# Performance work log

Hardware: AMD Instinct MI355X
Metric: run time of the kernel (lower is better)

The kernel has to match this reference:

```python
import jax, jax.numpy as jnp
import numpy as np

B, S, D = 2, 2048, 2048
H, D_NOPE, D_ROPE, D_V = 16, 128, 64, 128
R_Q, R_KV = 1536, 512
EPS = 1e-5


def _rmsnorm(x, w):
    return x * jax.lax.rsqrt(jnp.mean(x * x, axis=-1, keepdims=True) + EPS) * w


def setup_inputs() -> dict:
    key = jax.random.key(0)
    ks = jax.random.split(key, 12)
    x = jax.random.normal(ks[0], (B, S, D), jnp.float32)
    mask = jnp.zeros((B, 1, S, S), jnp.float32)  # unused by forward (is_causal)
    # NOTE: source apply_rope indexes freqs by HEAD axis -> shape (H, D_ROPE//2)
    ang = jax.random.uniform(ks[1], (H, D_ROPE // 2), jnp.float32) * (2.0 * np.pi)
    freqs_cos = jnp.cos(ang)
    freqs_sin = jnp.sin(ang)

    def lin(k, fan_in, fan_out):
        return jax.random.normal(k, (fan_in, fan_out), jnp.float32) * (fan_in ** -0.5)

    return {
        "x": x, "mask": mask, "freqs_cos": freqs_cos, "freqs_sin": freqs_sin,
        "w_cq": lin(ks[2], D, R_Q),
        "q_norm_w": jnp.ones((R_Q,), jnp.float32),
        "w_dq_nope": lin(ks[3], R_Q, H * D_NOPE),
        "w_dq_rope": lin(ks[4], R_Q, H * D_ROPE),
        "w_ckv": lin(ks[5], D, R_KV),
        "kv_norm_w": jnp.ones((R_KV,), jnp.float32),
        "w_dk_nope": lin(ks[6], R_KV, H * D_NOPE),
        "w_dv": lin(ks[7], R_KV, H * D_V),
        "w_k_rope": lin(ks[8], D, D_ROPE),
        "w_proj": lin(ks[9], H * D_V, D),
    }


def _apply_rope(q, k, cos, sin):
    # q: [B,H,S,Dr], k: [B,1,S,Dr]; cos/sin: [H, Dr/2] -> broadcast over head axis
    c = cos[None, :, None, :]
    s = sin[None, :, None, :]

    def rot(t):
        tr = t.reshape(t.shape[:-1] + (-1, 2))
        r, i = tr[..., 0], tr[..., 1]
        out_r = r * c - i * s  # k broadcasts from 1 head to H heads here
        out_i = r * s + i * c
        out = jnp.stack([out_r, out_i], axis=-1)
        return out.reshape(out.shape[:-2] + (-1,))

    return rot(q), rot(k)


def reference(x, mask, freqs_cos, freqs_sin, w_cq, q_norm_w, w_dq_nope, w_dq_rope,
              w_ckv, kv_norm_w, w_dk_nope, w_dv, w_k_rope, w_proj):
    b, s, _ = x.shape
    h = freqs_cos.shape[0]
    d_rope = freqs_cos.shape[1] * 2
    d_nope = w_dq_nope.shape[1] // h
    d_v = w_dv.shape[1] // h

    nq = _rmsnorm(x @ w_cq, q_norm_w)                      # [b,s,Rq]
    q_nope = (nq @ w_dq_nope).reshape(b, s, h, d_nope).transpose(0, 2, 1, 3)
    q_rope = (nq @ w_dq_rope).reshape(b, s, h, d_rope).transpose(0, 2, 1, 3)

    nkv = _rmsnorm(x @ w_ckv, kv_norm_w)                   # [b,s,Rkv]
    k_nope = (nkv @ w_dk_nope).reshape(b, s, h, d_nope).transpose(0, 2, 1, 3)
    v = (nkv @ w_dv).reshape(b, s, h, d_v).transpose(0, 2, 1, 3)
    v = v * (1.0 / jnp.sqrt(jnp.float32(h * d_v)))         # source scales V, not QK

    k_rope = (x @ w_k_rope).reshape(b, s, 1, d_rope).transpose(0, 2, 1, 3)
    q_rope, k_rope = _apply_rope(q_rope, k_rope, freqs_cos, freqs_sin)

    q = jnp.concatenate([q_nope, q_rope], axis=-1)         # [b,h,s,dn+dr]
    k = jnp.concatenate([k_nope, k_rope], axis=-1)

    attn_scale = 1.0 / jnp.sqrt(jnp.float32(d_nope + d_rope))  # SDPA default scale
    scores = jnp.einsum('bhqd,bhkd->bhqk', q, k) * attn_scale
    causal = jnp.tril(jnp.ones((s, s), dtype=bool))
    scores = jnp.where(causal[None, None], scores, -jnp.inf)
    probs = jax.nn.softmax(scores, axis=-1)

    out = jnp.einsum('bhqk,bhkd->bhqd', probs, v)
    out = out.transpose(0, 2, 1, 3).reshape(b, s, h * d_v)
    return out @ w_proj
```

## Files before the change

### kernel.cpp

```cpp
#include <hip/hip_runtime.h>
#include <hip/hip_bf16.h>
#include <cmath>
#include <cstdint>

using bf16 = __hip_bfloat16;
typedef __attribute__((ext_vector_type(8))) short short8;
typedef __attribute__((ext_vector_type(4))) float f32x4;

#define DEVINL static __device__ __forceinline__

DEVINL float bf2f(bf16 x) { return __bfloat162float(x); }
DEVINL bf16  f2bf(float x) { return __float2bfloat16(x); }
DEVINL unsigned short bfbits(float x) {
  bf16 h = __float2bfloat16(x);
  unsigned short u; __builtin_memcpy(&u, &h, 2); return u;
}
DEVINL float u2f(unsigned short u) {
  bf16 h; __builtin_memcpy(&h, &u, 2); return __bfloat162float(h);
}

typedef __attribute__((address_space(3))) void       lds_v;
typedef __attribute__((address_space(1))) const void gbl_v;
DEVINL void async16(const bf16* g, bf16* lds) {
  __builtin_amdgcn_global_load_lds((gbl_v*)g, (lds_v*)lds, 16, 0, 0);
}

template<int BM, int BN, int WM, int WN, bool OUT_BF16>
__global__ __launch_bounds__(256)
void gemm_bt(const bf16* __restrict__ A, const bf16* __restrict__ Bt,
             void* __restrict__ Cv, int M, int N, int K, float scale)
{
  constexpr int BK = 32;
  constexpr int FM = WM / 16, FN = WN / 16;
  constexpr int WAVES_N = BN / WN;
  __shared__ __align__(16) bf16 As[BM * BK];
  __shared__ __align__(16) bf16 Bs[BN * BK];

  const int tid = threadIdx.x, wid = tid >> 6, lane = tid & 63;
  const int nx = gridDim.x;
  const int nwg = nx * gridDim.y;
  const int bid0 = blockIdx.y * nx + blockIdx.x;
  const int cpx = nwg >> 3;
  const int swz = (bid0 & 7) * cpx + (bid0 >> 3);
  const int m0 = (swz / nx) * BM, n0 = (swz % nx) * BN;
  const int wm = wid / WAVES_N, wn = wid % WAVES_N;
  const int g = lane >> 4, l15 = lane & 15;
  const int srow = lane >> 2, schk = lane & 3;

  f32x4 acc[FM][FN] = {};

  for (int k0 = 0; k0 < K; k0 += BK) {
#pragma unroll
    for (int i = 0; i < BM / 64; i++) {
      int issue = wid * (BM / 64) + i;
      const bf16* src = A + (size_t)(m0 + issue * 16 + srow) * K + k0 + schk * 8;
      async16(src, (bf16*)As + issue * 512);
    }
#pragma unroll
    for (int i = 0; i < BN / 64; i++) {
      int issue = wid * (BN / 64) + i;
      const bf16* src = Bt + (size_t)(n0 + issue * 16 + srow) * K + k0 + schk * 8;
      async16(src, (bf16*)Bs + issue * 512);
    }
    __syncthreads();

    short8 af[FM], bfv[FN];
#pragma unroll
    for (int mi = 0; mi < FM; mi++)
      af[mi] = *(const short8*)&As[(wm * WM + mi * 16 + l15) * BK + g * 8];
#pragma unroll
    for (int ni = 0; ni < FN; ni++)
      bfv[ni] = *(const short8*)&Bs[(wn * WN + ni * 16 + l15) * BK + g * 8];
#pragma unroll
    for (int mi = 0; mi < FM; mi++)
#pragma unroll
      for (int ni = 0; ni < FN; ni++)
        acc[mi][ni] = __builtin_amdgcn_mfma_f32_16x16x32_bf16(af[mi], bfv[ni], acc[mi][ni], 0, 0, 0);
    __syncthreads();
  }

#pragma unroll
  for (int mi = 0; mi < FM; mi++)
#pragma unroll
    for (int ni = 0; ni < FN; ni++)
#pragma unroll
      for (int r = 0; r < 4; r++) {
        int row = m0 + wm * WM + mi * 16 + g * 4 + r;
        int col = n0 + wn * WN + ni * 16 + l15;
        float v = acc[mi][ni][r] * scale;
        if constexpr (OUT_BF16) ((bf16*)Cv)[(size_t)row * N + col] = f2bf(v);
        else                    ((float*)Cv)[(size_t)row * N + col] = v;
      }
}

struct TD { const float* src; bf16* dst; int R, C, start; float scale; };
struct TP8 { TD d[8]; };

__global__ void transpose_all_kernel(TP8 p)
{
  __shared__ float t[32][33];
  const int bid = blockIdx.x;
  int wi = 0;
#pragma unroll
  for (int i = 1; i < 8; i++) if (bid >= p.d[i].start) wi = i;
  const float* src = p.d[wi].src;
  bf16* dst = p.d[wi].dst;
  const int R = p.d[wi].R, C = p.d[wi].C;
  const float sc = p.d[wi].scale;
  const int local = bid - p.d[wi].start;
  const int ntx = C >> 5;
  const int bx = local % ntx, by = local / ntx;
  const int c0 = bx * 32, r0 = by * 32;
  const int tx = threadIdx.x, ty = threadIdx.y;
#pragma unroll
  for (int i = 0; i < 4; i++)
    t[ty + i * 8][tx] = src[(size_t)(r0 + ty + i * 8) * C + c0 + tx];
  __syncthreads();
#pragma unroll
  for (int i = 0; i < 4; i++)
    dst[(size_t)(c0 + ty + i * 8) * R + r0 + tx] = f2bf(t[tx][ty + i * 8] * sc);
}

__global__ void cast_kernel(const float* __restrict__ in, bf16* __restrict__ out, int n)
{
  int i = (blockIdx.x * 256 + threadIdx.x) * 4;
  if (i < n) {
    float4 v = *(const float4*)(in + i);
    ushort4 o;
    o.x = bfbits(v.x); o.y = bfbits(v.y); o.z = bfbits(v.z); o.w = bfbits(v.w);
    *reinterpret_cast<ushort4*>(out + i) = o;
  }
}

template<int NC>
__global__ __launch_bounds__(256)
void rmsnorm_kernel(const bf16* __restrict__ in, int stride, const float* __restrict__ w,
                    bf16* __restrict__ out)
{
  const int row = blockIdx.x;
  const bf16* x = in + (size_t)row * stride;
  float vals[NC / 256];
  float ssq = 0.f;
#pragma unroll
  for (int j = 0; j < NC / 512; j++) {
    int col = threadIdx.x * 2 + j * 512;
    ushort2 u = *reinterpret_cast<const ushort2*>(x + col);
    float a = u2f(u.x), c = u2f(u.y);
    vals[2 * j] = a; vals[2 * j + 1] = c;
    ssq += a * a + c * c;
  }
#pragma unroll
  for (int off = 32; off; off >>= 1) ssq += __shfl_xor(ssq, off, 64);
  __shared__ float red[4];
  const int wid = threadIdx.x >> 6, lane = threadIdx.x & 63;
  if (lane == 0) red[wid] = ssq;
  __syncthreads();
  float tot = red[0] + red[1] + red[2] + red[3];
  float sc = rsqrtf(tot * (1.f / NC) + 1e-5f);
#pragma unroll
  for (int j = 0; j < NC / 512; j++) {
    int col = threadIdx.x * 2 + j * 512;
    ushort2 o;
    o.x = bfbits(vals[2 * j] * sc * w[col]);
    o.y = bfbits(vals[2 * j + 1] * sc * w[col + 1]);
    *reinterpret_cast<ushort2*>(out + (size_t)row * NC + col) = o;
  }
}

__global__ void vtrans_kernel(const bf16* __restrict__ v, bf16* __restrict__ vt)
{
  __shared__ bf16 t[32][33];
  const int bh = blockIdx.z;
  const int s0 = blockIdx.x * 32, d0 = blockIdx.y * 32;
  const int tx = threadIdx.x, ty = threadIdx.y;
#pragma unroll
  for (int i = 0; i < 4; i++) {
    int s = s0 + ty + i * 8;
    t[ty + i * 8][tx] = v[((size_t)(bh >> 4) * 2048 + s) * 4096 + 2048 + (bh & 15) * 128 + d0 + tx];
  }
  __syncthreads();
#pragma unroll
  for (int i = 0; i < 4; i++)
    vt[((size_t)bh * 128 + d0 + ty + i * 8) * 2048 + s0 + tx] = t[tx][ty + i * 8];
}

__global__ __launch_bounds__(256, 2)
void flash_kernel(const bf16* __restrict__ qnr, const bf16* __restrict__ knb,
                  const bf16* __restrict__ krb, const bf16* __restrict__ vt,
                  bf16* __restrict__ o)
{
  constexpr int S = 2048, H = 16;
  constexpr int QSTR = 3072, KSTR = 4096, RSTR = 2112;
  const float SCALE = 0.07216878364870323f;
  const int bid = blockIdx.x;
  const int xcd = bid & 7, j = bid >> 3;
  const int slot = j & 31, rnd = j >> 5;
  const int grp = 4 * xcd + (slot >> 3);
  const int p = slot & 7;
  const int qti = rnd ? p : 15 - p;
  const int h = grp & 15, b = grp >> 4;
  const int q0 = qti * 128;

  const int tid = threadIdx.x, wid = tid >> 6, lane = tid & 63;
  const int g = lane >> 4, l15 = lane & 15;
  const int r4 = lane >> 4, s16 = lane & 15;
  const int r8 = lane >> 3, s8 = lane & 7;

  __shared__ __align__(16) bf16 KnS[2][64 * 128];
  __shared__ __align__(16) bf16 VtS[2][128 * 64];
  __shared__ __align__(16) bf16 KrS[64 * 64];
  __shared__ __align__(16) bf16 PS[4][16 * 64];

  short8 qf[2][6];
#pragma unroll
  for (int mi = 0; mi < 2; mi++) {
    int qrow = q0 + wid * 32 + mi * 16 + l15;
    const bf16* qnp = qnr + (size_t)(b * S + qrow) * QSTR + h * 128;
#pragma unroll
    for (int t = 0; t < 4; t++) qf[mi][t] = *(const short8*)(qnp + t * 32 + g * 8);
    const bf16* qrp = qnr + (size_t)(b * S + qrow) * QSTR + 2048 + h * 64;
#pragma unroll
    for (int t = 0; t < 2; t++) qf[mi][4 + t] = *(const short8*)(qrp + t * 32 + g * 8);
  }

  f32x4 oacc[2][8] = {};
  float mrow[2][4], lrow[2][4];
#pragma unroll
  for (int mi = 0; mi < 2; mi++)
#pragma unroll
    for (int r = 0; r < 4; r++) { mrow[mi][r] = -INFINITY; lrow[mi][r] = 0.f; }

  auto stage_knvt = [&](int kt, int buf) {
    const int k0s = kt * 64;
#pragma unroll
    for (int i = 0; i < 4; i++) {
      int issue = wid * 4 + i;
      int row = issue * 4 + r4;
      async16(knb + (size_t)(b * S + k0s + row) * KSTR + h * 128 + ((s16 ^ (row & 7)) * 8),
              &KnS[buf][issue * 512]);
    }
#pragma unroll
    for (int i = 0; i < 4; i++) {
      int issue = wid * 4 + i;
      int row = issue * 8 + r8;
      async16(vt + (((size_t)b * H + h) * 128 + row) * S + k0s + ((s8 ^ (row & 7)) * 8),
              &VtS[buf][issue * 512]);
    }
  };
  auto stage_kr = [&](int kt) {
    const int k0s = kt * 64;
#pragma unroll
    for (int i = 0; i < 2; i++) {
      int issue = wid * 2 + i;
      int row = issue * 8 + r8;
      async16(krb + (size_t)(b * S + k0s + row) * RSTR + 2048 + ((s8 ^ (row & 7)) * 8),
              &KrS[issue * 512]);
    }
  };

  const int niter = 2 * qti + 2;
  stage_knvt(0, 0);
  stage_kr(0);
  __syncthreads();

  int cb = 0;
  for (int kt = 0; kt < niter; kt++) {
    const int k0 = kt * 64;
    const bool pre = (kt + 1 < niter);
    if (pre) stage_knvt(kt + 1, cb ^ 1);

    const int base = q0 + wid * 32;
    const bool do0 = (k0 <= base + 15);
    const bool do1 = (k0 <= base + 31);

    f32x4 sacc[2][4] = {};
    if (do1) {
#pragma unroll
      for (int nt = 0; nt < 4; nt++) {
        int krow = nt * 16 + l15;
        int sw = krow & 7;
#pragma unroll
        for (int t = 0; t < 4; t++) {
          short8 kf = *(const short8*)&KnS[cb][krow * 128 + (((t * 4 + g) ^ sw) << 3)];
          sacc[0][nt] = __builtin_amdgcn_mfma_f32_16x16x32_bf16(qf[0][t], kf, sacc[0][nt], 0, 0, 0);
          sacc[1][nt] = __builtin_amdgcn_mfma_f32_16x16x32_bf16(qf[1][t], kf, sacc[1][nt], 0, 0, 0);
        }
#pragma unroll
        for (int t = 4; t < 6; t++) {
          short8 kf = *(const short8*)&KrS[krow * 64 + ((((t - 4) * 4 + g) ^ sw) << 3)];
          sacc[0][nt] = __builtin_amdgcn_mfma_f32_16x16x32_bf16(qf[0][t], kf, sacc[0][nt], 0, 0, 0);
          sacc[1][nt] = __builtin_amdgcn_mfma_f32_16x16x32_bf16(qf[1][t], kf, sacc[1][nt], 0, 0, 0);
        }
      }
    }
    __syncthreads();
    if (pre) stage_kr(kt + 1);

#pragma unroll
    for (int mi = 0; mi < 2; mi++) {
      if (!(mi ? do1 : do0)) continue;
      const int mrow0 = base + mi * 16;
      float pv[4][4];
      float mt[4] = {-INFINITY, -INFINITY, -INFINITY, -INFINITY};
      const bool diag = (k0 + 63 > mrow0);
#pragma unroll
      for (int nt = 0; nt < 4; nt++) {
        int key = k0 + nt * 16 + l15;
#pragma unroll
        for (int r = 0; r < 4; r++) {
          float v = sacc[mi][nt][r] * SCALE;
          int qrow = mrow0 + g * 4 + r;
          if (diag && key > qrow) v = -INFINITY;
          pv[nt][r] = v;
          mt[r] = fmaxf(mt[r], v);
        }
      }
#pragma unroll
      for (int r = 0; r < 4; r++)
#pragma unroll
        for (int off = 1; off < 16; off <<= 1)
          mt[r] = fmaxf(mt[r], __shfl_xor(mt[r], off, 64));

      float alpha[4], rs[4];
#pragma unroll
      for (int r = 0; r < 4; r++) {
        float mnew = fmaxf(mrow[mi][r], mt[r]);
        alpha[r] = __expf(mrow[mi][r] - mnew);
        mrow[mi][r] = mnew;
        rs[r] = 0.f;
      }
#pragma unroll
      for (int nt = 0; nt < 4; nt++)
#pragma unroll
        for (int r = 0; r < 4; r++) {
          float pe = __expf(pv[nt][r] - mrow[mi][r]);
          pv[nt][r] = pe;
          rs[r] += pe;
        }
#pragma unroll
      for (int r = 0; r < 4; r++) {
#pragma unroll
        for (int off = 1; off < 16; off <<= 1) rs[r] += __shfl_xor(rs[r], off, 64);
        lrow[mi][r] = lrow[mi][r] * alpha[r] + rs[r];
      }
#pragma unroll
      for (int f = 0; f < 8; f++)
#pragma unroll
        for (int r = 0; r < 4; r++) oacc[mi][f][r] *= alpha[r];

#pragma unroll
      for (int nt = 0; nt < 4; nt++)
#pragma unroll
        for (int r = 0; r < 4; r++) {
          int prow = g * 4 + r;
          int key = nt * 16 + l15;
          PS[wid][prow * 64 + (((key >> 3) ^ (prow & 7)) << 3) + (key & 7)] = f2bf(pv[nt][r]);
        }
      asm volatile("s_waitcnt lgkmcnt(0)" ::: "memory");
      __builtin_amdgcn_sched_barrier(0);

#pragma unroll
      for (int ks = 0; ks < 2; ks++) {
        short8 pf = *(const short8*)&PS[wid][l15 * 64 + ((((ks * 4 + g)) ^ (l15 & 7)) << 3)];
#pragma unroll
        for (int nt = 0; nt < 8; nt++) {
          int dv = nt * 16 + l15;
          short8 vf = *(const short8*)&VtS[cb][dv * 64 + ((((ks * 4 + g)) ^ (dv & 7)) << 3)];
          oacc[mi][nt] = __builtin_amdgcn_mfma_f32_16x16x32_bf16(pf, vf, oacc[mi][nt], 0, 0, 0);
        }
      }
    }
    __syncthreads();
    cb ^= 1;
  }

#pragma unroll
  for (int mi = 0; mi < 2; mi++)
#pragma unroll
    for (int nt = 0; nt < 8; nt++)
#pragma unroll
      for (int r = 0; r < 4; r++) {
        int row = q0 + wid * 32 + mi * 16 + g * 4 + r;
        int dv = nt * 16 + l15;
        o[(((size_t)b * S + row) * H + h) * 128 + dv] = f2bf(oacc[mi][nt][r] / lrow[mi][r]);
      }
}

extern "C" void kernel_launch(void* const* d_in, const int* in_sizes, int n_in,
                              void* d_out, int out_size, void* d_ws, size_t ws_size,
                              hipStream_t stream)
{
  (void)in_sizes; (void)n_in; (void)out_size; (void)ws_size;
  const float* x         = (const float*)d_in[0];
  const float* w_cq      = (const float*)d_in[4];
  const float* q_norm_w  = (const float*)d_in[5];
  const float* w_dq_nope = (const float*)d_in[6];
  const float* w_dq_rope = (const float*)d_in[7];
  const float* w_ckv     = (const float*)d_in[8];
  const float* kv_norm_w = (const float*)d_in[9];
  const float* w_dk_nope = (const float*)d_in[10];
  const float* w_dv      = (const float*)d_in[11];
  const float* w_k_rope  = (const float*)d_in[12];
  const float* w_proj    = (const float*)d_in[13];
  float* out = (float*)d_out;

  char* ws = (char*)d_ws;
  size_t off = 0;
  auto alloc = [&](size_t elems, size_t esz) -> void* {
    void* p = ws + off;
    off += (elems * esz + 255) & ~(size_t)255;
    return p;
  };
  bf16* xb     = (bf16*)alloc(8388608, 2);
  bf16* wTx    = (bf16*)alloc(4325376, 2);
  bf16* wTdq   = (bf16*)alloc(4718592, 2);
  bf16* wTdkv  = (bf16*)alloc(2097152, 2);
  bf16* wTproj = (bf16*)alloc(4194304, 2);
  bf16* g1     = (bf16*)alloc(8650752, 2);
  bf16* nq     = (bf16*)alloc(6291456, 2);
  bf16* nkv    = (bf16*)alloc(2097152, 2);
  bf16* g2     = (bf16*)alloc(12582912, 2);
  bf16* g3     = (bf16*)alloc(16777216, 2);
  bf16* vt     = (bf16*)alloc(8388608, 2);
  bf16* ao     = (bf16*)alloc(8388608, 2);

  cast_kernel<<<8192, 256, 0, stream>>>(x, xb, 8388608);

  const float SV = 0.022097086912079608f;
  TP8 tp;
  tp.d[0] = { w_cq,      wTx,                2048, 1536,     0, 1.f };
  tp.d[1] = { w_ckv,     wTx + 1536 * 2048,  2048, 512,   3072, 1.f };
  tp.d[2] = { w_k_rope,  wTx + 2048 * 2048,  2048, 64,    4096, 1.f };
  tp.d[3] = { w_dq_nope, wTdq,               1536, 2048,  4224, 1.f };
  tp.d[4] = { w_dq_rope, wTdq + 2048 * 1536, 1536, 1024,  7296, 1.f };
  tp.d[5] = { w_dk_nope, wTdkv,              512,  2048,  8832, 1.f };
  tp.d[6] = { w_dv,      wTdkv + 2048 * 512, 512,  2048,  9856, SV  };
  tp.d[7] = { w_proj,    wTproj,             2048, 2048, 10880, 1.f };
  transpose_all_kernel<<<14976, dim3(32, 8), 0, stream>>>(tp);

  gemm_bt<128, 64, 64, 32, true><<<dim3(33, 32), 256, 0, stream>>>(xb, wTx, g1, 4096, 2112, 2048, 1.f);

  rmsnorm_kernel<1536><<<4096, 256, 0, stream>>>(g1,        2112, q_norm_w,  nq);
  rmsnorm_kernel<512><<<4096, 256, 0, stream>>>(g1 + 1536,  2112, kv_norm_w, nkv);

  gemm_bt<128, 128, 64, 64, true><<<dim3(24, 32), 256, 0, stream>>>(nq,  wTdq,  g2, 4096, 3072, 1536, 1.f);
  gemm_bt<128, 128, 64, 64, true><<<dim3(32, 32), 256, 0, stream>>>(nkv, wTdkv, g3, 4096, 4096, 512, 1.f);

  vtrans_kernel<<<dim3(64, 4, 32), dim3(32, 8), 0, stream>>>(g3, vt);

  flash_kernel<<<512, 256, 0, stream>>>(g2, g3, g1, vt, ao);

  gemm_bt<128, 128, 64, 64, false><<<dim3(16, 32), 256, 0, stream>>>(ao, wTproj, out, 4096, 2048, 2048, 1.f);
}
```

Before: 532.6 us.

## Split causal attention KV range in two halves and merge partial results

Each query tile's key range is split into two halves handled by separate blocks, which doubles the grid to 1024 blocks. Each block writes an unnormalized bf16 partial output plus its row max and sum, and a new merge kernel combines the two with a log-sum-exp rescale. This replaces the previous heavy/light tile pairing and is meant to improve load balance and occupancy across CUs. In exchange it adds an extra kernel launch and extra global traffic for the partials, rounds the unnormalized partials to bf16, and reuses the xb and wTdkv workspace buffers as scratch.

```diff
diff --git a/kernel.cpp b/kernel.cpp
--- a/kernel.cpp
+++ b/kernel.cpp
@@ -187,19 +187,23 @@
 __global__ __launch_bounds__(256, 2)
 void flash_kernel(const bf16* __restrict__ qnr, const bf16* __restrict__ knb,
                   const bf16* __restrict__ krb, const bf16* __restrict__ vt,
-                  bf16* __restrict__ o)
+                  bf16* __restrict__ U, float* __restrict__ ML)
 {
   constexpr int S = 2048, H = 16;
   constexpr int QSTR = 3072, KSTR = 4096, RSTR = 2112;
   const float SCALE = 0.07216878364870323f;
   const int bid = blockIdx.x;
   const int xcd = bid & 7, j = bid >> 3;
-  const int slot = j & 31, rnd = j >> 5;
-  const int grp = 4 * xcd + (slot >> 3);
-  const int p = slot & 7;
-  const int qti = rnd ? p : 15 - p;
+  const int grp = 4 * xcd + (j >> 5);
+  const int sub = j & 31;
+  const int qti = 15 - (sub >> 1);
+  const int half = sub & 1;
   const int h = grp & 15, b = grp >> 4;
   const int q0 = qti * 128;
+  const int unit = (grp << 4) + qti;
+
+  const int kt0 = half ? (qti + 1) : 0;
+  const int kt1 = half ? (2 * qti + 2) : (qti + 1);
 
   const int tid = threadIdx.x, wid = tid >> 6, lane = tid & 63;
   const int g = lane >> 4, l15 = lane & 15;
@@ -258,15 +262,14 @@
     }
   };
 
-  const int niter = 2 * qti + 2;
-  stage_knvt(0, 0);
-  stage_kr(0);
+  stage_knvt(kt0, 0);
+  stage_kr(kt0);
   __syncthreads();
 
   int cb = 0;
-  for (int kt = 0; kt < niter; kt++) {
+  for (int kt = kt0; kt < kt1; kt++) {
     const int k0 = kt * 64;
-    const bool pre = (kt + 1 < niter);
+    const bool pre = (kt + 1 < kt1);
     if (pre) stage_knvt(kt + 1, cb ^ 1);
 
     const int base = q0 + wid * 32;
@@ -374,16 +377,60 @@
     cb ^= 1;
   }
 
-#pragma unroll
-  for (int mi = 0; mi < 2; mi++)
+  bf16* Up = U + (size_t)(unit * 2 + half) * 16384;
+  float* MLp = ML + (size_t)(unit * 2 + half) * 256;
+#pragma unroll
+  for (int mi = 0; mi < 2; mi++) {
 #pragma unroll
     for (int nt = 0; nt < 8; nt++)
 #pragma unroll
       for (int r = 0; r < 4; r++) {
-        int row = q0 + wid * 32 + mi * 16 + g * 4 + r;
+        int lr = wid * 32 + mi * 16 + g * 4 + r;
         int dv = nt * 16 + l15;
-        o[(((size_t)b * S + row) * H + h) * 128 + dv] = f2bf(oacc[mi][nt][r] / lrow[mi][r]);
-      }
+        Up[lr * 128 + dv] = f2bf(oacc[mi][nt][r]);
+      }
+    if (l15 == 0) {
+#pragma unroll
+      for (int r = 0; r < 4; r++) {
+        int lr = wid * 32 + mi * 16 + g * 4 + r;
+        MLp[lr] = mrow[mi][r];
+        MLp[128 + lr] = lrow[mi][r];
+      }
+    }
+  }
+}
+
+__global__ __launch_bounds__(256)
+void merge_kernel(const bf16* __restrict__ U, const float* __restrict__ ML,
+                  bf16* __restrict__ ao)
+{
+  const int u = blockIdx.x;
+  const int b = u >> 8, h = (u >> 4) & 15, qti = u & 15;
+  const int tid = threadIdx.x;
+  const int r = tid >> 1, d0 = (tid & 1) * 64;
+
+  const float m1 = ML[(size_t)u * 512 + r],       l1 = ML[(size_t)u * 512 + 128 + r];
+  const float m2 = ML[(size_t)u * 512 + 256 + r], l2 = ML[(size_t)u * 512 + 384 + r];
+  const float m = fmaxf(m1, m2);
+  const float a1 = __expf(m1 - m), a2 = __expf(m2 - m);
+  const float rl = 1.f / (a1 * l1 + a2 * l2);
+  const float s1 = a1 * rl, s2 = a2 * rl;
+
+  const bf16* U1 = U + (size_t)(u * 2) * 16384 + r * 128 + d0;
+  const bf16* U2 = U + (size_t)(u * 2 + 1) * 16384 + r * 128 + d0;
+  bf16* op = ao + (size_t)(b * 2048 + qti * 128 + r) * 2048 + h * 128 + d0;
+#pragma unroll
+  for (int j = 0; j < 64; j += 8) {
+    short8 v1 = *(const short8*)(U1 + j);
+    short8 v2 = *(const short8*)(U2 + j);
+    short8 o;
+#pragma unroll
+    for (int e = 0; e < 8; e++) {
+      float f = s1 * u2f((unsigned short)v1[e]) + s2 * u2f((unsigned short)v2[e]);
+      o[e] = (short)bfbits(f);
+    }
+    *(short8*)(op + j) = o;
+  }
 }
 
 extern "C" void kernel_launch(void* const* d_in, const int* in_sizes, int n_in,
@@ -424,6 +471,9 @@
   bf16* vt     = (bf16*)alloc(8388608, 2);
   bf16* ao     = (bf16*)alloc(8388608, 2);
 
+  bf16*  pU  = xb;
+  float* pML = (float*)wTdkv;
+
   cast_kernel<<<8192, 256, 0, stream>>>(x, xb, 8388608);
 
   const float SV = 0.022097086912079608f;
@@ -448,7 +498,8 @@
 
   vtrans_kernel<<<dim3(64, 4, 32), dim3(32, 8), 0, stream>>>(g3, vt);
 
-  flash_kernel<<<512, 256, 0, stream>>>(g2, g3, g1, vt, ao);
+  flash_kernel<<<1024, 256, 0, stream>>>(g2, g3, g1, vt, pU, pML);
+  merge_kernel<<<512, 256, 0, stream>>>(pU, pML, ao);
 
   gemm_bt<128, 128, 64, 64, false><<<dim3(16, 32), 256, 0, stream>>>(ao, wTproj, out, 4096, 2048, 2048, 1.f);
 }
```

New measurement: 545.3 us. 1.02x slower.
